# Performance work log

Hardware: AMD Instinct MI355X
Metric: run time of the kernel (lower is better)

## Reference

```python
import jax, jax.numpy as jnp
import numpy as np

EPS = 1e-6
H, KV, HD = 16, 4, 64      # q heads, kv heads, head dim
BLK = 32                   # dllm_block_length (block-diffusion attention)
TOPK = 2                   # experts per token

def rmsnorm(x, w):
    return x * jax.lax.rsqrt(jnp.mean(x * x, axis=-1, keepdims=True) + EPS) * w

def rotate_half(x):
    x1, x2 = jnp.split(x, 2, axis=-1)
    return jnp.concatenate([-x2, x1], axis=-1)

def setup_inputs() -> dict:
    key = jax.random.key(0)
    ks = jax.random.split(key, 12)
    B, S, D = 1, 2048, 1024
    E, I = 8, 1024
    s = 0.02
    pos = jnp.arange(S, dtype=jnp.float32)
    inv_freq = 1.0 / (10000.0 ** (jnp.arange(0, HD, 2, dtype=jnp.float32) / HD))
    emb = jnp.concatenate([jnp.outer(pos, inv_freq)] * 2, axis=-1)  # [S, HD]
    return {
        'hidden_states': jax.random.normal(ks[0], (B, S, D), jnp.float32),
        'cos': jnp.cos(emb), 'sin': jnp.sin(emb),
        'w_qkv': jax.random.normal(ks[1], (D, (H + 2 * KV) * HD), jnp.float32) * s,
        'w_o': jax.random.normal(ks[2], (H * HD, D), jnp.float32) * s,
        'q_norm_w': jnp.ones((HD,), jnp.float32),
        'k_norm_w': jnp.ones((HD,), jnp.float32),
        'in_ln_w': jnp.ones((D,), jnp.float32),
        'post_ln_w': jnp.ones((D,), jnp.float32),
        'router_w': jax.random.normal(ks[3], (D, E), jnp.float32) * s,
        'w_gate': jax.random.normal(ks[4], (E, D, I), jnp.float32) * s,
        'w_up': jax.random.normal(ks[5], (E, D, I), jnp.float32) * s,
        'w_down': jax.random.normal(ks[6], (E, I, D), jnp.float32) * s,
        'ws_gate': jax.random.normal(ks[7], (D, I), jnp.float32) * s,
        'ws_up': jax.random.normal(ks[8], (D, I), jnp.float32) * s,
        'ws_down': jax.random.normal(ks[9], (I, D), jnp.float32) * s,
    }

def reference(hidden_states, cos, sin, w_qkv, w_o, q_norm_w, k_norm_w, in_ln_w,
              post_ln_w, router_w, w_gate, w_up, w_down, ws_gate, ws_up, ws_down):
    B, S, D = hidden_states.shape
    scale = HD ** -0.5
    # --- attention (pre-norm) ---
    h = rmsnorm(hidden_states, in_ln_w)
    qkv = h @ w_qkv
    q, k, v = jnp.split(qkv, [H * HD, (H + KV) * HD], axis=-1)
    q = q.reshape(B, S, H, HD); k = k.reshape(B, S, KV, HD); v = v.reshape(B, S, KV, HD)
    q = rmsnorm(q, q_norm_w); k = rmsnorm(k, k_norm_w)   # qk-norm per head
    c = cos[None, :, None, :]; sn = sin[None, :, None, :]
    q = q * c + rotate_half(q) * sn
    k = k * c + rotate_half(k) * sn
    rep = H // KV
    k = jnp.repeat(k, rep, axis=2); v = jnp.repeat(v, rep, axis=2)  # GQA expand
    scores = jnp.einsum('bqhd,bkhd->bhqk', q, k) * scale
    blk = jnp.arange(S) // BLK
    mask = blk[:, None] >= blk[None, :]   # block-causal: full attn inside block
    scores = jnp.where(mask[None, None], scores, jnp.float32(-1e30))
    p = jax.nn.softmax(scores, axis=-1)
    attn = jnp.einsum('bhqk,bkhd->bqhd', p, v).reshape(B, S, H * HD)
    x = hidden_states + attn @ w_o
    # --- MoE FFN (pre-norm) ---
    h2 = rmsnorm(x, post_ln_w)
    t = h2.reshape(B * S, D)
    logits = t.astype(jnp.float32) @ router_w.astype(jnp.float32)  # fp32 router
    probs = jax.nn.softmax(logits, axis=-1)
    topv, topi = jax.lax.top_k(probs, TOPK)
    topv = topv / jnp.sum(topv, axis=-1, keepdims=True)            # norm_topk_prob
    E = router_w.shape[1]
    w_tok = jnp.zeros((t.shape[0], E), jnp.float32).at[
        jnp.arange(t.shape[0])[:, None], topi].set(topv).astype(t.dtype)
    g = jnp.einsum('td,edi->tei', t, w_gate)
    u = jnp.einsum('td,edi->tei', t, w_up)
    eo = jnp.einsum('tei,eid->ted', jax.nn.silu(g) * u, w_down)
    moe = jnp.einsum('te,ted->td', w_tok, eo)
    shared = (jax.nn.silu(t @ ws_gate) * (t @ ws_up)) @ ws_down
    return x + (moe + shared).reshape(B, S, D)
```

## Files before the change

kernel.cpp:

```cpp
#include <hip/hip_runtime.h>
#include <hip/hip_bf16.h>
#include <math.h>

#define S 2048
#define D 1024
#define NH 16
#define NKV 4
#define HD 64
#define QKV_N 1536
#define NE 8
#define NI 1024
#define EPS 1e-6f

typedef __bf16 bf16_t;
typedef __bf16 __attribute__((may_alias)) abf16;
typedef __attribute__((ext_vector_type(8))) __bf16 bf16x8;
typedef __attribute__((ext_vector_type(4))) float f32x4;
union I4B8 { int4 i; bf16x8 v; bf16_t e[8]; };

__device__ __forceinline__ void gll16(const void* g, void* l) {
  __builtin_amdgcn_global_load_lds(
      (const __attribute__((address_space(1))) void*)g,
      (__attribute__((address_space(3))) void*)l, 16, 0, 0);
}

__global__ void rmsnorm_kernel(const float* __restrict__ in, const float* __restrict__ w,
                               float* __restrict__ out32, __hip_bfloat16* __restrict__ out16) {
  int t = blockIdx.x;
  int tid = threadIdx.x;
  const float* row = in + (size_t)t * D;
  float v[4];
  float ss = 0.f;
#pragma unroll
  for (int i = 0; i < 4; ++i) {
    v[i] = row[tid + i * 256];
    ss += v[i] * v[i];
  }
#pragma unroll
  for (int off = 32; off; off >>= 1) ss += __shfl_xor(ss, off);
  __shared__ float wsum[4];
  int wave = tid >> 6;
  if ((tid & 63) == 0) wsum[wave] = ss;
  __syncthreads();
  float tot = wsum[0] + wsum[1] + wsum[2] + wsum[3];
  float r = rsqrtf(tot / (float)D + EPS);
#pragma unroll
  for (int i = 0; i < 4; ++i) {
    int d = tid + i * 256;
    float val = v[i] * r * w[d];
    if (out32) out32[(size_t)t * D + d] = val;
    if (out16) out16[(size_t)t * D + d] = __float2bfloat16(val);
  }
}

__global__ void transpose_cast_kernel(const float* __restrict__ W,
                                      __hip_bfloat16* __restrict__ WT, int Kd, int Nd) {
  __shared__ float tile[32][33];
  int e = blockIdx.z;
  const float* Wp = W + (size_t)e * Kd * Nd;
  __hip_bfloat16* WTp = WT + (size_t)e * Kd * Nd;
  int n0 = blockIdx.x * 32, k0 = blockIdx.y * 32;
  int tx = threadIdx.x & 31, ty = threadIdx.x >> 5;
#pragma unroll
  for (int i = 0; i < 4; ++i)
    tile[ty + i * 8][tx] = Wp[(size_t)(k0 + ty + i * 8) * Nd + n0 + tx];
  __syncthreads();
#pragma unroll
  for (int i = 0; i < 4; ++i)
    WTp[(size_t)(n0 + ty + i * 8) * Kd + k0 + tx] = __float2bfloat16(tile[tx][ty + i * 8]);
}

__global__ void v_transpose_kernel(const float* __restrict__ qkv, __hip_bfloat16* __restrict__ vT) {
  __shared__ float tile[32][33];
  int t0 = blockIdx.x * 32;
  int c0 = blockIdx.y * 32;
  int tx = threadIdx.x & 31, ty = threadIdx.x >> 5;
#pragma unroll
  for (int i = 0; i < 4; ++i)
    tile[ty + i * 8][tx] = qkv[(size_t)(t0 + ty + i * 8) * QKV_N + (NH + NKV) * HD + c0 + tx];
  __syncthreads();
#pragma unroll
  for (int i = 0; i < 4; ++i)
    vT[(size_t)(c0 + ty + i * 8) * S + t0 + tx] = __float2bfloat16(tile[tx][ty + i * 8]);
}

__global__ __launch_bounds__(256) void mgemm_kernel(
    const __hip_bfloat16* __restrict__ A, const __hip_bfloat16* __restrict__ BT,
    const float* __restrict__ Cadd, float* __restrict__ C,
    int M, int N, int K,
    const int* __restrict__ counts, const int* __restrict__ offsets,
    const int* __restrict__ tok, int a_comp,
    const __hip_bfloat16* __restrict__ As2, const __hip_bfloat16* __restrict__ BTs2,
    float* __restrict__ Cs2) {
  __shared__ __align__(16) bf16_t Asd[2][128 * 32];
  __shared__ __align__(16) bf16_t Bsd[2][128 * 32];
  __shared__ int rowmap[128];
  int e = blockIdx.z;
  bool sh = (counts != nullptr) && (e == NE);
  int cnt = sh ? M : (counts ? counts[e] : M);
  int bm = blockIdx.y * 128;
  if (bm >= cnt) return;
  int bn = blockIdx.x * 128;
  int obase = sh ? 0 : (offsets ? offsets[e] : 0);
  const bf16_t* Ab = sh ? (const bf16_t*)As2 : (const bf16_t*)A;
  const bf16_t* BTe = sh ? (const bf16_t*)BTs2 : ((const bf16_t*)BT + (size_t)e * N * K);
  float* Cp = sh ? Cs2 : C;
  const int* toke = (!sh && tok) ? tok + e * S : nullptr;
  int acompe = sh ? 0 : a_comp;
  int tid = threadIdx.x;
  if (tid < 128) {
    int gp = bm + tid;
    int cp = gp < cnt ? gp : cnt - 1;
    rowmap[tid] = toke ? toke[cp] : (acompe ? obase + cp : cp);
  }
  __syncthreads();
  int wave = tid >> 6, lane = tid & 63;
  int quad = lane >> 4, l16 = lane & 15;
  int wm = wave >> 1, wn = wave & 1;
  int srow = tid >> 2, scol = (tid & 3) * 8;
  size_t aoff0 = (size_t)rowmap[srow] * K + scol;
  size_t aoff1 = (size_t)rowmap[64 + srow] * K + scol;
  size_t boff0 = (size_t)(bn + srow) * K + scol;
  size_t boff1 = (size_t)(bn + 64 + srow) * K + scol;
  f32x4 acc[4][4];
#pragma unroll
  for (int i = 0; i < 4; ++i)
#pragma unroll
    for (int j = 0; j < 4; ++j) acc[i][j] = (f32x4){0.f, 0.f, 0.f, 0.f};

  {
    char* AsB = (char*)Asd[0] + wave * 1024;
    char* BsB = (char*)Bsd[0] + wave * 1024;
    gll16(Ab + aoff0, AsB);
    gll16(Ab + aoff1, AsB + 4096);
    gll16(BTe + boff0, BsB);
    gll16(BTe + boff1, BsB + 4096);
  }
  for (int k0 = 0; k0 < K; k0 += 32) {
    int cur = (k0 >> 5) & 1;
    __syncthreads();
    if (k0 + 32 < K) {
      char* AsB = (char*)Asd[cur ^ 1] + wave * 1024;
      char* BsB = (char*)Bsd[cur ^ 1] + wave * 1024;
      gll16(Ab + aoff0 + k0 + 32, AsB);
      gll16(Ab + aoff1 + k0 + 32, AsB + 4096);
      gll16(BTe + boff0 + k0 + 32, BsB);
      gll16(BTe + boff1 + k0 + 32, BsB + 4096);
    }
    I4B8 af[4], bfr[4];
#pragma unroll
    for (int i = 0; i < 4; ++i)
      af[i].i = *(const int4*)(Asd[cur] + (wm * 64 + i * 16 + l16) * 32 + quad * 8);
#pragma unroll
    for (int j = 0; j < 4; ++j)
      bfr[j].i = *(const int4*)(Bsd[cur] + (wn * 64 + j * 16 + l16) * 32 + quad * 8);
#pragma unroll
    for (int i = 0; i < 4; ++i)
#pragma unroll
      for (int j = 0; j < 4; ++j)
        acc[i][j] = __builtin_amdgcn_mfma_f32_16x16x32_bf16(af[i].v, bfr[j].v, acc[i][j], 0, 0, 0);
  }
#pragma unroll
  for (int i = 0; i < 4; ++i) {
#pragma unroll
    for (int r = 0; r < 4; ++r) {
      int trow = wm * 64 + i * 16 + quad * 4 + r;
      int gp = bm + trow;
      if (gp < cnt) {
        size_t rowb = (size_t)(obase + gp) * N;
#pragma unroll
        for (int j = 0; j < 4; ++j) {
          int col = bn + wn * 64 + j * 16 + l16;
          size_t idx = rowb + col;
          Cp[idx] = acc[i][j][r] + (Cadd ? Cadd[idx] : 0.f);
        }
      }
    }
  }
}

__global__ __launch_bounds__(256) void mgemm_gu_kernel(
    const __hip_bfloat16* __restrict__ A, const __hip_bfloat16* __restrict__ BTg,
    const __hip_bfloat16* __restrict__ BTu, __hip_bfloat16* __restrict__ act,
    int M, int N, int K,
    const int* __restrict__ counts, const int* __restrict__ offsets,
    const int* __restrict__ tok,
    const __hip_bfloat16* __restrict__ BTgs, const __hip_bfloat16* __restrict__ BTus,
    __hip_bfloat16* __restrict__ acts) {
  __shared__ __align__(16) bf16_t Asd[2][128 * 32];
  __shared__ __align__(16) bf16_t Bgd[2][64 * 32];
  __shared__ __align__(16) bf16_t Bud[2][64 * 32];
  __shared__ int rowmap[128];
  int e = blockIdx.z;
  bool sh = (counts != nullptr) && (e == NE);
  int cnt = sh ? M : (counts ? counts[e] : M);
  int bm = blockIdx.y * 128;
  if (bm >= cnt) return;
  int bn = blockIdx.x * 64;
  const bf16_t* Ab = (const bf16_t*)A;
  const bf16_t* Bg = sh ? (const bf16_t*)BTgs : ((const bf16_t*)BTg + (size_t)e * N * K);
  const bf16_t* Bu = sh ? (const bf16_t*)BTus : ((const bf16_t*)BTu + (size_t)e * N * K);
  bf16_t* outp = sh ? (bf16_t*)acts : (bf16_t*)act;
  int obase = sh ? 0 : (offsets ? offsets[e] : 0);
  const int* toke = (!sh && tok) ? tok + e * S : nullptr;
  int tid = threadIdx.x;
  if (tid < 128) {
    int gp = bm + tid;
    int cp = gp < cnt ? gp : cnt - 1;
    rowmap[tid] = toke ? toke[cp] : cp;
  }
  __syncthreads();
  int wave = tid >> 6, lane = tid & 63;
  int quad = lane >> 4, l16 = lane & 15;
  int wm = wave >> 1, wn = wave & 1;
  int srow = tid >> 2, scol = (tid & 3) * 8;
  size_t aoff0 = (size_t)rowmap[srow] * K + scol;
  size_t aoff1 = (size_t)rowmap[64 + srow] * K + scol;
  size_t boff = (size_t)(bn + srow) * K + scol;
  f32x4 accg[4][2], accu[4][2];
#pragma unroll
  for (int i = 0; i < 4; ++i)
#pragma unroll
    for (int j = 0; j < 2; ++j) {
      accg[i][j] = (f32x4){0.f, 0.f, 0.f, 0.f};
      accu[i][j] = (f32x4){0.f, 0.f, 0.f, 0.f};
    }
  {
    char* AsB = (char*)Asd[0] + wave * 1024;
    gll16(Ab + aoff0, AsB);
    gll16(Ab + aoff1, AsB + 4096);
    gll16(Bg + boff, (char*)Bgd[0] + wave * 1024);
    gll16(Bu + boff, (char*)Bud[0] + wave * 1024);
  }
  for (int k0 = 0; k0 < K; k0 += 32) {
    int cur = (k0 >> 5) & 1;
    __syncthreads();
    if (k0 + 32 < K) {
      char* AsB = (char*)Asd[cur ^ 1] + wave * 1024;
      gll16(Ab + aoff0 + k0 + 32, AsB);
      gll16(Ab + aoff1 + k0 + 32, AsB + 4096);
      gll16(Bg + boff + k0 + 32, (char*)Bgd[cur ^ 1] + wave * 1024);
      gll16(Bu + boff + k0 + 32, (char*)Bud[cur ^ 1] + wave * 1024);
    }
    I4B8 af[4], bg[2], bu[2];
#pragma unroll
    for (int i = 0; i < 4; ++i)
      af[i].i = *(const int4*)(Asd[cur] + (wm * 64 + i * 16 + l16) * 32 + quad * 8);
#pragma unroll
    for (int j = 0; j < 2; ++j) {
      bg[j].i = *(const int4*)(Bgd[cur] + (wn * 32 + j * 16 + l16) * 32 + quad * 8);
      bu[j].i = *(const int4*)(Bud[cur] + (wn * 32 + j * 16 + l16) * 32 + quad * 8);
    }
#pragma unroll
    for (int i = 0; i < 4; ++i)
#pragma unroll
      for (int j = 0; j < 2; ++j) {
        accg[i][j] = __builtin_amdgcn_mfma_f32_16x16x32_bf16(af[i].v, bg[j].v, accg[i][j], 0, 0, 0);
        accu[i][j] = __builtin_amdgcn_mfma_f32_16x16x32_bf16(af[i].v, bu[j].v, accu[i][j], 0, 0, 0);
      }
  }
#pragma unroll
  for (int i = 0; i < 4; ++i) {
#pragma unroll
    for (int r = 0; r < 4; ++r) {
      int trow = wm * 64 + i * 16 + quad * 4 + r;
      int gp = bm + trow;
      if (gp < cnt) {
        size_t rowb = (size_t)(obase + gp) * N;
#pragma unroll
        for (int j = 0; j < 2; ++j) {
          int col = bn + wn * 32 + j * 16 + l16;
          float g = accg[i][j][r], uu = accu[i][j][r];
          float sg = g / (1.f + __expf(-g));
          outp[rowb + col] = __float2bfloat16(sg * uu);
        }
      }
    }
  }
}

__global__ void qkv_post_kernel(const float* __restrict__ qkv,
                                const float* __restrict__ qw, const float* __restrict__ kw,
                                const float* __restrict__ cosb, const float* __restrict__ sinb,
                                __hip_bfloat16* __restrict__ qout,
                                __hip_bfloat16* __restrict__ kout,
                                __hip_bfloat16* __restrict__ vout) {
  int t = blockIdx.x;
  int u = blockIdx.y * 4 + (threadIdx.x >> 6);
  int lane = threadIdx.x & 63;
  if (u >= NH + NKV) {
    int h = u - NH - NKV;
    float xv = qkv[(size_t)t * QKV_N + (NH + NKV) * HD + h * HD + lane];
    vout[(size_t)t * (NKV * HD) + h * HD + lane] = __float2bfloat16(xv);
    return;
  }
  bool isq = (u < NH);
  int h = isq ? u : (u - NH);
  size_t src = (size_t)t * QKV_N + (isq ? (h * HD) : (NH * HD + h * HD)) + lane;
  float xv = qkv[src];
  float ss = xv * xv;
#pragma unroll
  for (int off = 32; off; off >>= 1) ss += __shfl_xor(ss, off);
  float r = rsqrtf(ss * (1.f / 64.f) + EPS);
  float xn = xv * r * (isq ? qw[lane] : kw[lane]);
  float other = __shfl_xor(xn, 32);
  float rot = (lane < 32) ? -other : other;
  float res = xn * cosb[t * 64 + lane] + rot * sinb[t * 64 + lane];
  if (isq) qout[(size_t)t * (NH * HD) + h * HD + lane] = __float2bfloat16(res * 0.125f);
  else     kout[(size_t)t * (NKV * HD) + h * HD + lane] = __float2bfloat16(res);
}

__global__ __launch_bounds__(256) void attn_kernel(
    const __hip_bfloat16* __restrict__ qg, const __hip_bfloat16* __restrict__ kg,
    const __hip_bfloat16* __restrict__ vT,
    float* __restrict__ opart0, float* __restrict__ opart1,
    float* __restrict__ mpart, float* __restrict__ lpart) {
  int qt = (int)(gridDim.x - 1) - (int)blockIdx.x;
  int kvh = blockIdx.y;
  int z = blockIdx.z;
  int tid = threadIdx.x;
  int wave = tid >> 6, lane = tid & 63;
  int quad = lane >> 4, l16 = lane & 15;
  int h = kvh * 4 + wave;

  float* opz = z ? opart1 : opart0;
  float* mp = mpart + (size_t)z * S * NH;
  float* lp = lpart + (size_t)z * S * NH;

  int nb = (qt >> 1) + 1;
  int nt = (nb + 1) >> 1;
  bool halfm = (nb & 1) != 0;
  int h0 = nt >> 1;
  int lo = z ? h0 : 0;
  int hi = z ? nt : h0;

  if (lo >= hi) {
    int row = qt * 16 + (tid >> 4);
    float* od = opz + (size_t)row * (NH * HD) + kvh * 256 + (tid & 15) * 16;
    int4 zz = {0, 0, 0, 0};
#pragma unroll
    for (int i = 0; i < 4; ++i) *(int4*)(od + i * 4) = zz;
    if (tid < 64) {
      int rr = qt * 16 + (tid >> 2), hh = kvh * 4 + (tid & 3);
      mp[(size_t)rr * NH + hh] = -1e30f;
      lp[(size_t)rr * NH + hh] = 0.f;
    }
    return;
  }

  __shared__ __align__(16) int KsI[64 * 36];
  __shared__ __align__(16) int VTI[64 * 36];
  __shared__ __align__(16) int PsI[4][16 * 36];

  I4B8 qf[2];
#pragma unroll
  for (int ch = 0; ch < 2; ++ch)
    qf[ch].i = *(const int4*)((const abf16*)qg +
        (size_t)(qt * 16 + l16) * (NH * HD) + h * HD + ch * 32 + quad * 8);

  I4B8 ones;
  ones.i = (int4){0x3F803F80, 0x3F803F80, 0x3F803F80, 0x3F803F80};

  float m_r[4];
  f32x4 o[4], o4;
#pragma unroll
  for (int r = 0; r < 4; ++r) m_r[r] = -1e30f;
#pragma unroll
  for (int sub = 0; sub < 4; ++sub) o[sub] = (f32x4){0.f, 0.f, 0.f, 0.f};
  o4 = (f32x4){0.f, 0.f, 0.f, 0.f};

  int sp = tid >> 3, sc = tid & 7;
  const abf16* kb = (const abf16*)kg;
  const abf16* vb = (const abf16*)vT;

  int4 rk0 = *(const int4*)(kb + (size_t)(lo * 64 + sp) * (NKV * HD) + kvh * HD + sc * 8);
  int4 rk1 = *(const int4*)(kb + (size_t)(lo * 64 + 32 + sp) * (NKV * HD) + kvh * HD + sc * 8);
  int4 rv0 = *(const int4*)(vb + (size_t)(kvh * HD + sp) * S + lo * 64 + sc * 8);
  int4 rv1 = *(const int4*)(vb + (size_t)(kvh * HD + 32 + sp) * S + lo * 64 + sc * 8);

  for (int kc = lo; kc < hi; ++kc) {
    *(int4*)&KsI[sp * 36 + sc * 4] = rk0;
    *(int4*)&KsI[(sp + 32) * 36 + sc * 4] = rk1;
    *(int4*)&VTI[sp * 36 + sc * 4] = rv0;
    *(int4*)&VTI[(sp + 32) * 36 + sc * 4] = rv1;
    __syncthreads();

    if (kc + 1 < hi) {
      rk0 = *(const int4*)(kb + (size_t)((kc + 1) * 64 + sp) * (NKV * HD) + kvh * HD + sc * 8);
      rk1 = *(const int4*)(kb + (size_t)((kc + 1) * 64 + 32 + sp) * (NKV * HD) + kvh * HD + sc * 8);
      rv0 = *(const int4*)(vb + (size_t)(kvh * HD + sp) * S + (kc + 1) * 64 + sc * 8);
      rv1 = *(const int4*)(vb + (size_t)(kvh * HD + 32 + sp) * S + (kc + 1) * 64 + sc * 8);
    }

    f32x4 s[4];
#pragma unroll
    for (int sub = 0; sub < 4; ++sub) s[sub] = (f32x4){0.f, 0.f, 0.f, 0.f};
    __builtin_amdgcn_s_setprio(1);
#pragma unroll
    for (int sub = 0; sub < 4; ++sub)
#pragma unroll
      for (int ch = 0; ch < 2; ++ch) {
        I4B8 ku;
        ku.i = *(const int4*)&KsI[(sub * 16 + l16) * 36 + ch * 16 + quad * 4];
        s[sub] = __builtin_amdgcn_mfma_f32_16x16x32_bf16(qf[ch].v, ku.v, s[sub], 0, 0, 0);
      }
    __builtin_amdgcn_s_setprio(0);
    if (halfm && kc == nt - 1) {
#pragma unroll
      for (int r = 0; r < 4; ++r) { s[2][r] = -1e30f; s[3][r] = -1e30f; }
    }

    abf16* pw = (abf16*)PsI[wave];
#pragma unroll
    for (int r = 0; r < 4; ++r) {
      float v = fmaxf(fmaxf(s[0][r], s[1][r]), fmaxf(s[2][r], s[3][r]));
#pragma unroll
      for (int off = 1; off < 16; off <<= 1) v = fmaxf(v, __shfl_xor(v, off));
      float mx = fmaxf(m_r[r], v);
      float al = __expf(m_r[r] - mx);
      m_r[r] = mx;
      float p0 = __expf(s[0][r] - mx);
      float p1 = __expf(s[1][r] - mx);
      float p2 = __expf(s[2][r] - mx);
      float p3 = __expf(s[3][r] - mx);
      int prow = quad * 4 + r;
      pw[prow * 72 + l16]      = (bf16_t)p0;
      pw[prow * 72 + 16 + l16] = (bf16_t)p1;
      pw[prow * 72 + 32 + l16] = (bf16_t)p2;
      pw[prow * 72 + 48 + l16] = (bf16_t)p3;
      o4[r] *= al;
#pragma unroll
      for (int sub = 0; sub < 4; ++sub) o[sub][r] *= al;
    }

    I4B8 pu[2];
#pragma unroll
    for (int ch = 0; ch < 2; ++ch)
      pu[ch].i = *(const int4*)&PsI[wave][l16 * 36 + ch * 16 + quad * 4];
    __builtin_amdgcn_s_setprio(1);
#pragma unroll
    for (int sub = 0; sub < 4; ++sub)
#pragma unroll
      for (int ch = 0; ch < 2; ++ch) {
        I4B8 vf;
        vf.i = *(const int4*)&VTI[(sub * 16 + l16) * 36 + ch * 16 + quad * 4];
        o[sub] = __builtin_amdgcn_mfma_f32_16x16x32_bf16(pu[ch].v, vf.v, o[sub], 0, 0, 0);
      }
#pragma unroll
    for (int ch = 0; ch < 2; ++ch)
      o4 = __builtin_amdgcn_mfma_f32_16x16x32_bf16(pu[ch].v, ones.v, o4, 0, 0, 0);
    __builtin_amdgcn_s_setprio(0);
    __syncthreads();
  }

#pragma unroll
  for (int r = 0; r < 4; ++r) {
    int row = qt * 16 + quad * 4 + r;
    float* od = opz + (size_t)row * (NH * HD) + h * HD;
#pragma unroll
    for (int sub = 0; sub < 4; ++sub)
      od[sub * 16 + l16] = o[sub][r];
    if (l16 == 0) {
      mp[(size_t)row * NH + h] = m_r[r];
      lp[(size_t)row * NH + h] = o4[r];
    }
  }
}

__global__ void attn_merge_kernel(const float* __restrict__ opart0,
                                  const float* __restrict__ opart1,
                                  const float* __restrict__ mpart,
                                  const float* __restrict__ lpart,
                                  __hip_bfloat16* __restrict__ attn) {
  int row = blockIdx.x;
  int tid = threadIdx.x;
#pragma unroll
  for (int i = 0; i < 4; ++i) {
    int c = tid + i * 256;
    int h = c >> 6;
    float m0 = mpart[(size_t)row * NH + h];
    float m1 = mpart[(size_t)(S + row) * NH + h];
    float l0 = lpart[(size_t)row * NH + h];
    float l1 = lpart[(size_t)(S + row) * NH + h];
    float M = fmaxf(m0, m1);
    float a0 = __expf(m0 - M), a1 = __expf(m1 - M);
    float l = l0 * a0 + l1 * a1;
    float v = (opart0[(size_t)row * (NH * HD) + c] * a0 +
               opart1[(size_t)row * (NH * HD) + c] * a1) / l;
    attn[(size_t)row * (NH * HD) + c] = __float2bfloat16(v);
  }
}

__global__ void router_kernel(const float* __restrict__ h2, const float* __restrict__ rw,
                              int* __restrict__ topk_e, float* __restrict__ topk_w) {
  int t = blockIdx.x * 4 + (threadIdx.x >> 6);
  int lane = threadIdx.x & 63;
  float p[NE] = {};
  for (int d = lane; d < D; d += 64) {
    float hv = h2[(size_t)t * D + d];
#pragma unroll
    for (int e = 0; e < NE; ++e) p[e] += hv * rw[d * NE + e];
  }
#pragma unroll
  for (int off = 32; off; off >>= 1)
#pragma unroll
    for (int e = 0; e < NE; ++e) p[e] += __shfl_xor(p[e], off);
  if (lane == 0) {
    float mx = p[0];
#pragma unroll
    for (int e = 1; e < NE; ++e) mx = fmaxf(mx, p[e]);
    float ex[NE];
#pragma unroll
    for (int e = 0; e < NE; ++e) ex[e] = __expf(p[e] - mx);
    int e0 = 0;
#pragma unroll
    for (int e = 1; e < NE; ++e) if (ex[e] > ex[e0]) e0 = e;
    int e1 = (e0 == 0) ? 1 : 0;
#pragma unroll
    for (int e = 0; e < NE; ++e) if (e != e0 && ex[e] > ex[e1]) e1 = e;
    float w0 = ex[e0] / (ex[e0] + ex[e1]);
    float w1 = ex[e1] / (ex[e0] + ex[e1]);
    topk_e[2 * t] = e0;  topk_e[2 * t + 1] = e1;
    topk_w[2 * t] = w0;  topk_w[2 * t + 1] = w1;
  }
}

__global__ __launch_bounds__(1024) void router_place_kernel(
    const int* __restrict__ topk_e, int* __restrict__ counts, int* __restrict__ offsets,
    int* __restrict__ tok_list, int* __restrict__ topk_pos) {
  __shared__ int lcnt[NE];
  int tid = threadIdx.x;
  int lane = tid & 63;
  if (tid < NE) lcnt[tid] = 0;
  __syncthreads();
#pragma unroll
  for (int r = 0; r < 2; ++r) {
    int t = r * 1024 + tid;
#pragma unroll
    for (int s = 0; s < 2; ++s) {
      int e = topk_e[2 * t + s];
      int pos = 0;
#pragma unroll
      for (int x = 0; x < NE; ++x) {
        unsigned long long mask = __ballot(e == x);
        if (mask) {
          int leader = __ffsll((unsigned long long)mask) - 1;
          int cnt = __popcll(mask);
          int base = 0;
          if (lane == leader) base = atomicAdd(&lcnt[x], cnt);
          base = __shfl(base, leader);
          if (e == x)
            pos = base + __popcll(mask & ((1ull << lane) - 1ull));
        }
      }
      topk_pos[2 * t + s] = pos;
      tok_list[e * S + pos] = t;
    }
  }
  __syncthreads();
  if (tid == 0) {
    int acc = 0;
    for (int e = 0; e < NE; ++e) { offsets[e] = acc; counts[e] = lcnt[e]; acc += lcnt[e]; }
  }
}

__global__ void final_kernel(const float* __restrict__ x, const float* __restrict__ sout,
                             const float* __restrict__ eo,
                             const int* __restrict__ topk_e, const int* __restrict__ topk_pos,
                             const float* __restrict__ topk_w, const int* __restrict__ offsets,
                             float* __restrict__ out) {
  int t = blockIdx.x;
  int tid = threadIdx.x;
  int e0 = topk_e[2 * t], e1 = topk_e[2 * t + 1];
  size_t r0 = (size_t)offsets[e0] + topk_pos[2 * t];
  size_t r1 = (size_t)offsets[e1] + topk_pos[2 * t + 1];
  float w0 = topk_w[2 * t], w1 = topk_w[2 * t + 1];
#pragma unroll
  for (int i = 0; i < 4; ++i) {
    int d = tid + i * 256;
    size_t idx = (size_t)t * D + d;
    out[idx] = x[idx] + sout[idx] + w0 * eo[r0 * D + d] + w1 * eo[r1 * D + d];
  }
}

extern "C" void kernel_launch(void* const* d_in, const int* in_sizes, int n_in,
                              void* d_out, int out_size, void* d_ws, size_t ws_size,
                              hipStream_t stream) {
  const float* hidden  = (const float*)d_in[0];
  const float* cosb    = (const float*)d_in[1];
  const float* sinb    = (const float*)d_in[2];
  const float* w_qkv   = (const float*)d_in[3];
  const float* w_o     = (const float*)d_in[4];
  const float* q_norm  = (const float*)d_in[5];
  const float* k_norm  = (const float*)d_in[6];
  const float* in_ln   = (const float*)d_in[7];
  const float* post_ln = (const float*)d_in[8];
  const float* router_w= (const float*)d_in[9];
  const float* w_gate  = (const float*)d_in[10];
  const float* w_up    = (const float*)d_in[11];
  const float* w_down  = (const float*)d_in[12];
  const float* ws_gate = (const float*)d_in[13];
  const float* ws_up   = (const float*)d_in[14];
  const float* ws_down = (const float*)d_in[15];
  float* out = (float*)d_out;
  float* ws = (float*)d_ws;

  typedef __hip_bfloat16 hbf;
  hbf* wqkvT = (hbf*)(ws);
  hbf* woT   = (hbf*)(ws +  768 * 1024);
  hbf* wgT   = (hbf*)(ws + 1280 * 1024);
  hbf* wuT   = (hbf*)(ws + 5376 * 1024);
  hbf* wdT   = (hbf*)(ws + 9472 * 1024);
  hbf* wsgT  = (hbf*)(ws + 13568 * 1024);
  hbf* wsuT  = (hbf*)(ws + 14080 * 1024);
  hbf* wsdT  = (hbf*)(ws + 14592 * 1024);
  hbf*   hb      = (hbf*)(ws + 15104 * 1024);
  float* qkv     = ws + 16128 * 1024;
  hbf*   qbB     = (hbf*)(ws + 19200 * 1024);
  hbf*   kbB     = (hbf*)(ws + 20224 * 1024);
  hbf*   vTb     = (hbf*)(ws + 20480 * 1024);
  hbf*   attnb16 = (hbf*)(ws + 20736 * 1024);
  float* x       = ws + 22784 * 1024;
  float* h2      = ws + 24832 * 1024;
  hbf*   h2b     = (hbf*)(ws + 26880 * 1024);
  hbf*   act     = (hbf*)(ws + 16128 * 1024);
  float* eo      = ws + 18176 * 1024;
  hbf*   sact    = (hbf*)(ws + 27904 * 1024);
  float* sout    = ws + 28928 * 1024;
  float* mpart   = ws + 15104 * 1024;
  float* lpart   = mpart + 2 * S * NH;
  float* opart0  = ws + 16128 * 1024;
  float* opart1  = ws + 22784 * 1024;
  int* counts   = (int*)(ws + 30976 * 1024);
  int* offsets  = counts + NE;
  int* tok_list = offsets + NE;
  int* topk_e   = tok_list + NE * S;
  int* topk_pos = topk_e + 2 * S;
  float* topk_w = (float*)(topk_pos + 2 * S);

  dim3 b256(256);
  transpose_cast_kernel<<<dim3(QKV_N/32, D/32, 1), b256, 0, stream>>>(w_qkv, wqkvT, D, QKV_N);
  transpose_cast_kernel<<<dim3(D/32, D/32, 1),     b256, 0, stream>>>(w_o, woT, D, D);
  transpose_cast_kernel<<<dim3(NI/32, D/32, NE),   b256, 0, stream>>>(w_gate, wgT, D, NI);
  transpose_cast_kernel<<<dim3(NI/32, D/32, NE),   b256, 0, stream>>>(w_up, wuT, D, NI);
  transpose_cast_kernel<<<dim3(D/32, NI/32, NE),   b256, 0, stream>>>(w_down, wdT, NI, D);
  transpose_cast_kernel<<<dim3(NI/32, D/32, 1),    b256, 0, stream>>>(ws_gate, wsgT, D, NI);
  transpose_cast_kernel<<<dim3(NI/32, D/32, 1),    b256, 0, stream>>>(ws_up, wsuT, D, NI);
  transpose_cast_kernel<<<dim3(D/32, NI/32, 1),    b256, 0, stream>>>(ws_down, wsdT, NI, D);
  rmsnorm_kernel<<<S, b256, 0, stream>>>(hidden, in_ln, nullptr, hb);
  mgemm_kernel<<<dim3(QKV_N/128, S/128, 1), b256, 0, stream>>>(hb, wqkvT, nullptr, qkv,
      S, QKV_N, D, nullptr, nullptr, nullptr, 0, nullptr, nullptr, nullptr);
  qkv_post_kernel<<<dim3(S, 5), b256, 0, stream>>>(qkv, q_norm, k_norm, cosb, sinb, qbB, kbB, nullptr);
  v_transpose_kernel<<<dim3(S/32, (NKV*HD)/32), b256, 0, stream>>>(qkv, vTb);
  attn_kernel<<<dim3(S/16, NKV, 2), b256, 0, stream>>>(qbB, kbB, vTb,
      opart0, opart1, mpart, lpart);
  attn_merge_kernel<<<S, b256, 0, stream>>>(opart0, opart1, mpart, lpart, attnb16);
  mgemm_kernel<<<dim3(D/128, S/128, 1), b256, 0, stream>>>(attnb16, woT, hidden, x,
      S, D, D, nullptr, nullptr, nullptr, 0, nullptr, nullptr, nullptr);
  rmsnorm_kernel<<<S, b256, 0, stream>>>(x, post_ln, h2, h2b);
  router_kernel<<<S/4, b256, 0, stream>>>(h2, router_w, topk_e, topk_w);
  router_place_kernel<<<1, 1024, 0, stream>>>(topk_e, counts, offsets, tok_list, topk_pos);
  mgemm_gu_kernel<<<dim3(NI/64, S/128, NE + 1), b256, 0, stream>>>(h2b, wgT, wuT, act,
      S, NI, D, counts, offsets, tok_list, wsgT, wsuT, sact);
  mgemm_kernel<<<dim3(D/128, S/128, NE + 1), b256, 0, stream>>>(act, wdT, nullptr, eo,
      S, D, NI, counts, offsets, nullptr, 1, sact, wsdT, sout);
  final_kernel<<<S, b256, 0, stream>>>(x, sout, eo, topk_e, topk_pos, topk_w, offsets, out);
}
```

Before: 444.8 us.

## Triple-buffer LDS tiles in MoE GEMM kernels with explicit vmcnt waits

Moves both grouped GEMM kernels (plain and fused gate/up) from double-buffered to triple-buffered LDS staging, prefetching two K-tiles ahead. Explicit s_waitcnt vmcnt(4) plus a raw s_barrier replace __syncthreads, so the next tile's loads can stay in flight while the current tile is consumed. This is meant to hide global-load latency behind MFMA work. In exchange LDS use per block rises by half, which may reduce occupancy, and correctness now depends on the hand-counted vmcnt value matching the four loads issued per stage.

```diff
diff --git a/kernel.cpp b/kernel.cpp
--- a/kernel.cpp
+++ b/kernel.cpp
@@ -92,8 +92,8 @@
     const int* __restrict__ tok, int a_comp,
     const __hip_bfloat16* __restrict__ As2, const __hip_bfloat16* __restrict__ BTs2,
     float* __restrict__ Cs2) {
-  __shared__ __align__(16) bf16_t Asd[2][128 * 32];
-  __shared__ __align__(16) bf16_t Bsd[2][128 * 32];
+  __shared__ __align__(16) bf16_t Asd[3][128 * 32];
+  __shared__ __align__(16) bf16_t Bsd[3][128 * 32];
   __shared__ int rowmap[128];
   int e = blockIdx.z;
   bool sh = (counts != nullptr) && (e == NE);
@@ -128,6 +128,7 @@
 #pragma unroll
     for (int j = 0; j < 4; ++j) acc[i][j] = (f32x4){0.f, 0.f, 0.f, 0.f};
 
+  int nt = K >> 5;
   {
     char* AsB = (char*)Asd[0] + wave * 1024;
     char* BsB = (char*)Bsd[0] + wave * 1024;
@@ -135,30 +136,46 @@
     gll16(Ab + aoff1, AsB + 4096);
     gll16(BTe + boff0, BsB);
     gll16(BTe + boff1, BsB + 4096);
-  }
-  for (int k0 = 0; k0 < K; k0 += 32) {
-    int cur = (k0 >> 5) & 1;
-    __syncthreads();
-    if (k0 + 32 < K) {
-      char* AsB = (char*)Asd[cur ^ 1] + wave * 1024;
-      char* BsB = (char*)Bsd[cur ^ 1] + wave * 1024;
-      gll16(Ab + aoff0 + k0 + 32, AsB);
-      gll16(Ab + aoff1 + k0 + 32, AsB + 4096);
-      gll16(BTe + boff0 + k0 + 32, BsB);
-      gll16(BTe + boff1 + k0 + 32, BsB + 4096);
-    }
+    if (nt > 1) {
+      char* AsB1 = (char*)Asd[1] + wave * 1024;
+      char* BsB1 = (char*)Bsd[1] + wave * 1024;
+      gll16(Ab + aoff0 + 32, AsB1);
+      gll16(Ab + aoff1 + 32, AsB1 + 4096);
+      gll16(BTe + boff0 + 32, BsB1);
+      gll16(BTe + boff1 + 32, BsB1 + 4096);
+    }
+  }
+  int cur = 0;
+  for (int t = 0; t < nt; ++t) {
+    if (t == nt - 1) asm volatile("s_waitcnt vmcnt(0)" ::: "memory");
+    else             asm volatile("s_waitcnt vmcnt(4)" ::: "memory");
+    __builtin_amdgcn_s_barrier();
+    asm volatile("" ::: "memory");
+    if (t + 2 < nt) {
+      int pb = cur + 2; if (pb >= 3) pb -= 3;
+      int kp = (t + 2) << 5;
+      char* AsB = (char*)Asd[pb] + wave * 1024;
+      char* BsB = (char*)Bsd[pb] + wave * 1024;
+      gll16(Ab + aoff0 + kp, AsB);
+      gll16(Ab + aoff1 + kp, AsB + 4096);
+      gll16(BTe + boff0 + kp, BsB);
+      gll16(BTe + boff1 + kp, BsB + 4096);
+    }
+    const bf16_t* Ac = Asd[cur];
+    const bf16_t* Bc = Bsd[cur];
     I4B8 af[4], bfr[4];
 #pragma unroll
     for (int i = 0; i < 4; ++i)
-      af[i].i = *(const int4*)(Asd[cur] + (wm * 64 + i * 16 + l16) * 32 + quad * 8);
+      af[i].i = *(const int4*)(Ac + (wm * 64 + i * 16 + l16) * 32 + quad * 8);
 #pragma unroll
     for (int j = 0; j < 4; ++j)
-      bfr[j].i = *(const int4*)(Bsd[cur] + (wn * 64 + j * 16 + l16) * 32 + quad * 8);
+      bfr[j].i = *(const int4*)(Bc + (wn * 64 + j * 16 + l16) * 32 + quad * 8);
 #pragma unroll
     for (int i = 0; i < 4; ++i)
 #pragma unroll
       for (int j = 0; j < 4; ++j)
         acc[i][j] = __builtin_amdgcn_mfma_f32_16x16x32_bf16(af[i].v, bfr[j].v, acc[i][j], 0, 0, 0);
+    cur = (cur == 2) ? 0 : cur + 1;
   }
 #pragma unroll
   for (int i = 0; i < 4; ++i) {
@@ -187,9 +204,9 @@
     const int* __restrict__ tok,
     const __hip_bfloat16* __restrict__ BTgs, const __hip_bfloat16* __restrict__ BTus,
     __hip_bfloat16* __restrict__ acts) {
-  __shared__ __align__(16) bf16_t Asd[2][128 * 32];
-  __shared__ __align__(16) bf16_t Bgd[2][64 * 32];
-  __shared__ __align__(16) bf16_t Bud[2][64 * 32];
+  __shared__ __align__(16) bf16_t Asd[3][128 * 32];
+  __shared__ __align__(16) bf16_t Bgd[3][64 * 32];
+  __shared__ __align__(16) bf16_t Bud[3][64 * 32];
   __shared__ int rowmap[128];
   int e = blockIdx.z;
   bool sh = (counts != nullptr) && (e == NE);
@@ -225,31 +242,47 @@
       accg[i][j] = (f32x4){0.f, 0.f, 0.f, 0.f};
       accu[i][j] = (f32x4){0.f, 0.f, 0.f, 0.f};
     }
+  int nt = K >> 5;
   {
     char* AsB = (char*)Asd[0] + wave * 1024;
     gll16(Ab + aoff0, AsB);
     gll16(Ab + aoff1, AsB + 4096);
     gll16(Bg + boff, (char*)Bgd[0] + wave * 1024);
     gll16(Bu + boff, (char*)Bud[0] + wave * 1024);
-  }
-  for (int k0 = 0; k0 < K; k0 += 32) {
-    int cur = (k0 >> 5) & 1;
-    __syncthreads();
-    if (k0 + 32 < K) {
-      char* AsB = (char*)Asd[cur ^ 1] + wave * 1024;
-      gll16(Ab + aoff0 + k0 + 32, AsB);
-      gll16(Ab + aoff1 + k0 + 32, AsB + 4096);
-      gll16(Bg + boff + k0 + 32, (char*)Bgd[cur ^ 1] + wave * 1024);
-      gll16(Bu + boff + k0 + 32, (char*)Bud[cur ^ 1] + wave * 1024);
-    }
+    if (nt > 1) {
+      char* AsB1 = (char*)Asd[1] + wave * 1024;
+      gll16(Ab + aoff0 + 32, AsB1);
+      gll16(Ab + aoff1 + 32, AsB1 + 4096);
+      gll16(Bg + boff + 32, (char*)Bgd[1] + wave * 1024);
+      gll16(Bu + boff + 32, (char*)Bud[1] + wave * 1024);
+    }
+  }
+  int cur = 0;
+  for (int t = 0; t < nt; ++t) {
+    if (t == nt - 1) asm volatile("s_waitcnt vmcnt(0)" ::: "memory");
+    else             asm volatile("s_waitcnt vmcnt(4)" ::: "memory");
+    __builtin_amdgcn_s_barrier();
+    asm volatile("" ::: "memory");
+    if (t + 2 < nt) {
+      int pb = cur + 2; if (pb >= 3) pb -= 3;
+      int kp = (t + 2) << 5;
+      char* AsB = (char*)Asd[pb] + wave * 1024;
+      gll16(Ab + aoff0 + kp, AsB);
+      gll16(Ab + aoff1 + kp, AsB + 4096);
+      gll16(Bg + boff + kp, (char*)Bgd[pb] + wave * 1024);
+      gll16(Bu + boff + kp, (char*)Bud[pb] + wave * 1024);
+    }
+    const bf16_t* Ac = Asd[cur];
+    const bf16_t* Bgc = Bgd[cur];
+    const bf16_t* Buc = Bud[cur];
     I4B8 af[4], bg[2], bu[2];
 #pragma unroll
     for (int i = 0; i < 4; ++i)
-      af[i].i = *(const int4*)(Asd[cur] + (wm * 64 + i * 16 + l16) * 32 + quad * 8);
+      af[i].i = *(const int4*)(Ac + (wm * 64 + i * 16 + l16) * 32 + quad * 8);
 #pragma unroll
     for (int j = 0; j < 2; ++j) {
-      bg[j].i = *(const int4*)(Bgd[cur] + (wn * 32 + j * 16 + l16) * 32 + quad * 8);
-      bu[j].i = *(const int4*)(Bud[cur] + (wn * 32 + j * 16 + l16) * 32 + quad * 8);
+      bg[j].i = *(const int4*)(Bgc + (wn * 32 + j * 16 + l16) * 32 + quad * 8);
+      bu[j].i = *(const int4*)(Buc + (wn * 32 + j * 16 + l16) * 32 + quad * 8);
     }
 #pragma unroll
     for (int i = 0; i < 4; ++i)
@@ -258,6 +291,7 @@
         accg[i][j] = __builtin_amdgcn_mfma_f32_16x16x32_bf16(af[i].v, bg[j].v, accg[i][j], 0, 0, 0);
         accu[i][j] = __builtin_amdgcn_mfma_f32_16x16x32_bf16(af[i].v, bu[j].v, accu[i][j], 0, 0, 0);
       }
+    cur = (cur == 2) ? 0 : cur + 1;
   }
 #pragma unroll
   for (int i = 0; i < 4; ++i) {
```

Measured after the change: 442.9 us. About the same (-0.4%).
